# Optimization experiments

Hardware: AMD Instinct MI355X
Metric: run time of the kernel (lower is better)

The kernel has to match this reference:

```python
import jax, jax.numpy as jnp
import numpy as np

B, S, H = 4, 8192, 768
NH, HD = 12, 64          # num_heads, head_size
M = 64                   # projection_dim = min(256, HD)
EPS = 1e-6

def setup_inputs() -> dict:
    key = jax.random.key(0)
    ks = jax.random.split(key, 10)
    scale_w = 0.02
    scale_p = 1.0 / np.sqrt(HD)
    return {
        'hidden_states': jax.random.normal(ks[0], (B, S, H), jnp.float32),
        'Wq': jax.random.normal(ks[1], (H, H), jnp.float32) * scale_w,
        'bq': jnp.zeros((H,), jnp.float32),
        'Wk': jax.random.normal(ks[2], (H, H), jnp.float32) * scale_w,
        'bk': jnp.zeros((H,), jnp.float32),
        'Wv': jax.random.normal(ks[3], (H, H), jnp.float32) * scale_w,
        'bv': jnp.zeros((H,), jnp.float32),
        'Wo': jax.random.normal(ks[4], (H, H), jnp.float32) * scale_w,
        'bo': jnp.zeros((H,), jnp.float32),
        'projection_matrix': jax.random.normal(ks[5], (NH, HD, M), jnp.float32) * scale_p,
    }

def reference(hidden_states, Wq, bq, Wk, bk, Wv, bv, Wo, bo, projection_matrix):
    b, s, h = hidden_states.shape
    def heads(x):  # [b,s,h] -> [b,nh,s,hd]
        return x.reshape(b, s, NH, HD).transpose(0, 2, 1, 3)
    q = heads(hidden_states @ Wq + bq)
    k = heads(hidden_states @ Wk + bk)
    v = heads(hidden_states @ Wv + bv)
    # random-feature projection + stabilized exp feature map
    qp = jnp.einsum('bhnd,hdm->bhnm', q, projection_matrix)
    kp = jnp.einsum('bhnd,hdm->bhnm', k, projection_matrix)
    qp = jnp.exp(qp - jnp.max(qp, axis=-1, keepdims=True))
    kp = jnp.exp(kp - jnp.max(kp, axis=-1, keepdims=True))
    # O(n) linear attention: kv summary [b,h,m,hd]
    kv = jnp.einsum('bhnm,bhnd->bhmd', kp, v)
    qkv = jnp.einsum('bhnm,bhmd->bhnd', qp, kv)
    k_sum = jnp.sum(kp, axis=2)                      # [b,h,m]
    normalizer = jnp.einsum('bhnm,bhm->bhn', qp, k_sum)[..., None]
    ctx = qkv / (normalizer + EPS)
    ctx = ctx.transpose(0, 2, 1, 3).reshape(b, s, NH * HD)
    return ctx @ Wo + bo
```

## Files before the change

kernel.cpp:

```cpp
#include <hip/hip_runtime.h>
#include <hip/hip_bf16.h>


#define S_    8192
#define H_    768
#define NH_   12
#define EPS_  1e-6f

typedef unsigned short U16;
typedef short bf16x8 __attribute__((ext_vector_type(8)));
typedef float f32x4  __attribute__((ext_vector_type(4)));

__device__ __forceinline__ U16 f2b(float x) {
  unsigned u = __float_as_uint(x);
  return (U16)((u + 0x7fffu + ((u >> 16) & 1u)) >> 16);
}
__device__ __forceinline__ float b2f(U16 h) {
  return __uint_as_float(((unsigned)h) << 16);
}
__device__ __forceinline__ void gl2lds16(const void* g, void* l) {
  __builtin_amdgcn_global_load_lds(
      (const __attribute__((address_space(1))) void*)g,
      (__attribute__((address_space(3))) void*)l, 16, 0, 0);
}

__global__ void zero_f32(float* __restrict__ p, int n) {
  int i = blockIdx.x * 256 + threadIdx.x;
  if (i < n) p[i] = 0.f;
}

__global__ void cvt_f32_bf16(const float* __restrict__ src, U16* __restrict__ hi, int n4) {
  int i = blockIdx.x * 256 + threadIdx.x;
  if (i >= n4) return;
  float4 x = ((const float4*)src)[i];
  ushort4 h;
  h.x = f2b(x.x); h.y = f2b(x.y); h.z = f2b(x.z); h.w = f2b(x.w);
  ((ushort4*)hi)[i] = h;
}

__global__ void fold_proj(const float* __restrict__ Wq, const float* __restrict__ bq,
                          const float* __restrict__ Wk, const float* __restrict__ bk,
                          const float* __restrict__ P,
                          float* __restrict__ Wqp, float* __restrict__ bqp,
                          float* __restrict__ Wkp, float* __restrict__ bkp) {
  __shared__ float Pl[64 * 64];
  __shared__ float WL[4 * 64];
  int h = blockIdx.y, kc = blockIdx.x, tid = threadIdx.x;
  const float* W  = blockIdx.z ? Wk : Wq;
  const float* bb = blockIdx.z ? bk : bq;
  float* Wout = blockIdx.z ? Wkp : Wqp;
  float* bout = blockIdx.z ? bkp : bqp;
  const float4* P4 = (const float4*)(P + (size_t)h * 4096);
#pragma unroll
  for (int i = 0; i < 4; ++i) ((float4*)Pl)[tid + i * 256] = P4[tid + i * 256];
  WL[tid] = W[(size_t)(kc * 4 + (tid >> 6)) * H_ + h * 64 + (tid & 63)];
  __syncthreads();
  int kl = tid >> 6, m = tid & 63;
  float acc = 0.f;
#pragma unroll
  for (int d = 0; d < 64; ++d) acc += WL[kl * 64 + d] * Pl[d * 64 + m];
  Wout[(size_t)(kc * 4 + kl) * H_ + h * 64 + m] = acc;
  if (kc == 0 && tid < 64) {
    float a2 = 0.f;
    for (int d = 0; d < 64; ++d) a2 += bb[h * 64 + d] * Pl[d * 64 + tid];
    bout[h * 64 + tid] = a2;
  }
}

__global__ void build_cat(const float* __restrict__ Wqp, const float* __restrict__ Wkp,
                          const float* __restrict__ Wv,  const float* __restrict__ Wo,
                          U16* __restrict__ WcatH, U16* __restrict__ WoTH) {
  int k = blockIdx.x * 256 + threadIdx.x;
  int r = blockIdx.y;
  float v; U16* dh; size_t off;
  if (r < 768)       { v = Wqp[(size_t)k * H_ + r];          off = (size_t)r * H_ + k;          dh = WcatH; }
  else if (r < 1536) { v = Wkp[(size_t)k * H_ + (r - 768)];  off = (size_t)r * H_ + k;          dh = WcatH; }
  else if (r < 2304) { v = Wv [(size_t)k * H_ + (r - 1536)]; off = (size_t)r * H_ + k;          dh = WcatH; }
  else               { v = Wo [(size_t)k * H_ + (r - 2304)]; off = (size_t)(r - 2304) * H_ + k; dh = WoTH; }
  dh[off] = f2b(v);
}

__global__ void build_bias(const float* __restrict__ bqp, const float* __restrict__ bkp,
                           const float* __restrict__ bv, float* __restrict__ biasC) {
  int i = blockIdx.x * 256 + threadIdx.x;
  if (i >= 2304) return;
  biasC[i] = i < 768 ? bqp[i] : (i < 1536 ? bkp[i - 768] : bv[i - 1536]);
}

__global__ __launch_bounds__(256, 2) void gemm_qkv(
    const U16* __restrict__ Ahi, const U16* __restrict__ Bhi,
    const float* __restrict__ bias,
    U16* __restrict__ qp, U16* __restrict__ kpT, U16* __restrict__ vT) {
  __shared__ __align__(16) U16 Us[32768];
  const int tid = threadIdx.x, w = tid >> 6, lane = tid & 63;
  const int quad = lane >> 4, l16 = lane & 15;
  const int b = blockIdx.x;
  const int mt = b & 255, nt0 = b >> 8;
  const int rowA0 = mt * 128;
  const int wm = w & 1, wn = w >> 1;
  const U16* srcA[4];
  int rowBl[4];
  unsigned ldsc[4];
  const int kch = ((lane & 7) ^ (lane >> 3)) * 8;
#pragma unroll
  for (int t = 0; t < 4; ++t) {
    int c = w * 4 + t;
    int row = c * 8 + (lane >> 3);
    srcA[t] = Ahi + (size_t)(rowA0 + row) * H_ + kch;
    rowBl[t] = row;
    ldsc[t] = (unsigned)c * 512;
  }
  auto stage = [&](int jn, int tn, int bi) {
    const int colB = (nt0 + 2 * jn) * 128;
    unsigned ub = (unsigned)bi * 16384u;
#pragma unroll
    for (int t = 0; t < 4; ++t) {
      gl2lds16(srcA[t] + tn * 64, &Us[ub + ldsc[t]]);
      gl2lds16(Bhi + (size_t)(colB + rowBl[t]) * H_ + tn * 64 + kch,
               &Us[ub + 8192u + ldsc[t]]);
    }
  };

  stage(0, 0, 0);
  for (int jj = 0; jj < 9; ++jj) {
    const int colB0 = (nt0 + 2 * jj) * 128;
    f32x4 acc[4][4] = {};
    for (int t = 0; t < 12; ++t) {
      const bool more = !(jj == 8 && t == 11);
      if (more) {
        if (t < 11) stage(jj, t + 1, (t + 1) & 1);
        else        stage(jj + 1, 0, 0);
        asm volatile("s_waitcnt vmcnt(8)" ::: "memory");
      } else {
        asm volatile("s_waitcnt vmcnt(0)" ::: "memory");
      }
      __builtin_amdgcn_sched_barrier(0);
      __builtin_amdgcn_s_barrier();
      __builtin_amdgcn_sched_barrier(0);
      const unsigned ab = (unsigned)(t & 1) * 16384u;
      bf16x8 ah[4][2], bh[4][2];
#pragma unroll
      for (int i = 0; i < 4; ++i)
#pragma unroll
        for (int ks = 0; ks < 2; ++ks)
          ah[i][ks] = *(const bf16x8*)&Us[ab +
              (unsigned)((wm * 64 + i * 16 + l16) * 64 +
                         (((ks * 4 + quad) ^ (l16 & 7)) * 8))];
#pragma unroll
      for (int j = 0; j < 4; ++j)
#pragma unroll
        for (int ks = 0; ks < 2; ++ks)
          bh[j][ks] = *(const bf16x8*)&Us[ab + 8192u +
              (unsigned)((wn * 64 + j * 16 + l16) * 64 +
                         (((ks * 4 + quad) ^ (l16 & 7)) * 8))];
      asm volatile("s_waitcnt lgkmcnt(0)" ::: "memory");
      __builtin_amdgcn_sched_barrier(0);
      __builtin_amdgcn_s_setprio(1);
#pragma unroll
      for (int ks = 0; ks < 2; ++ks)
#pragma unroll
        for (int j = 0; j < 4; ++j)
#pragma unroll
          for (int i = 0; i < 4; ++i)
            acc[i][j] = __builtin_amdgcn_mfma_f32_16x16x32_bf16(
                ah[i][ks], bh[j][ks], acc[i][j], 0, 0, 0);
      __builtin_amdgcn_s_setprio(0);
      __builtin_amdgcn_sched_barrier(0);
      __builtin_amdgcn_s_barrier();
      __builtin_amdgcn_sched_barrier(0);
    }
    const int col64 = colB0 + wn * 64;
    float bj[4];
#pragma unroll
    for (int j = 0; j < 4; ++j) bj[j] = bias[col64 + j * 16 + l16];
    if (col64 < 768) {
      const int h = col64 >> 6;
#pragma unroll
      for (int i = 0; i < 4; ++i) {
#pragma unroll
        for (int r = 0; r < 4; ++r) {
          int row = rowA0 + wm * 64 + i * 16 + quad * 4 + r;
          float v0 = acc[i][0][r] + bj[0], v1 = acc[i][1][r] + bj[1];
          float v2 = acc[i][2][r] + bj[2], v3 = acc[i][3][r] + bj[3];
          float mx = fmaxf(fmaxf(v0, v1), fmaxf(v2, v3));
          mx = fmaxf(mx, __shfl_xor(mx, 1));
          mx = fmaxf(mx, __shfl_xor(mx, 2));
          mx = fmaxf(mx, __shfl_xor(mx, 4));
          mx = fmaxf(mx, __shfl_xor(mx, 8));
          int bb = row >> 13, s = row & 8191;
          size_t base = ((size_t)(bb * NH_ + h) * S_ + s) * 64 + l16;
          qp[base +  0] = f2b(__expf(v0 - mx));
          qp[base + 16] = f2b(__expf(v1 - mx));
          qp[base + 32] = f2b(__expf(v2 - mx));
          qp[base + 48] = f2b(__expf(v3 - mx));
        }
      }
    } else {
      const int isv = col64 >= 1536;
      const int h = (col64 - (isv ? 1536 : 768)) >> 6;
      U16* dstT = isv ? vT : kpT;
#pragma unroll
      for (int i = 0; i < 4; ++i) {
        float er[4][4];
#pragma unroll
        for (int r = 0; r < 4; ++r) {
          float v0 = acc[i][0][r] + bj[0], v1 = acc[i][1][r] + bj[1];
          float v2 = acc[i][2][r] + bj[2], v3 = acc[i][3][r] + bj[3];
          if (!isv) {
            float mx = fmaxf(fmaxf(v0, v1), fmaxf(v2, v3));
            mx = fmaxf(mx, __shfl_xor(mx, 1));
            mx = fmaxf(mx, __shfl_xor(mx, 2));
            mx = fmaxf(mx, __shfl_xor(mx, 4));
            mx = fmaxf(mx, __shfl_xor(mx, 8));
            v0 = __expf(v0 - mx); v1 = __expf(v1 - mx);
            v2 = __expf(v2 - mx); v3 = __expf(v3 - mx);
          }
          er[0][r] = v0; er[1][r] = v1; er[2][r] = v2; er[3][r] = v3;
        }
        int n = rowA0 + wm * 64 + i * 16 + quad * 4;
        int bb = n >> 13, s = n & 8191;
        int bh2 = bb * NH_ + h;
#pragma unroll
        for (int j = 0; j < 4; ++j) {
          ushort4 o;
          o.x = f2b(er[j][0]); o.y = f2b(er[j][1]);
          o.z = f2b(er[j][2]); o.w = f2b(er[j][3]);
          *(ushort4*)&dstT[((size_t)bh2 * 64 + j * 16 + l16) * S_ + s] = o;
        }
      }
    }
  }
}

__global__ __launch_bounds__(256, 4) void kv_accum_mfma(
    const U16* __restrict__ kpT, const U16* __restrict__ vT,
    float* __restrict__ kvT) {
  __shared__ __align__(16) U16 Us[2 * 64 * 64];
  const int tid = threadIdx.x, w = tid >> 6, lane = tid & 63;
  const int quad = lane >> 4, l16 = lane & 15;
  const int bh = blockIdx.y;
  const int n0 = blockIdx.x * 512;
  const U16* srcs[4];
  unsigned ldsoff[4];
#pragma unroll
  for (int t = 0; t < 4; ++t) {
    int c = w * 4 + t, buf = c >> 3;
    int r = (c & 7) * 8 + (lane >> 3);
    const U16* base = buf ? kpT : vT;
    srcs[t] = base + ((size_t)bh * 64 + r) * S_ + n0 + (lane & 7) * 8;
    ldsoff[t] = buf * 4096 + (c & 7) * 512;
  }
  f32x4 acc[4] = {};
  float ks[4] = {0.f, 0.f, 0.f, 0.f};
  for (int nc = 0; nc < 512; nc += 64) {
#pragma unroll
    for (int t = 0; t < 4; ++t) gl2lds16(srcs[t] + nc, &Us[ldsoff[t]]);
    __syncthreads();
#pragma unroll
    for (int k0 = 0; k0 < 64; k0 += 32) {
      bf16x8 av = *(const bf16x8*)&Us[(w * 16 + l16) * 64 + k0 + quad * 8];
#pragma unroll
      for (int j = 0; j < 4; ++j) {
        bf16x8 bk = *(const bf16x8*)&Us[4096 + (j * 16 + l16) * 64 + k0 + quad * 8];
        if (w == 0) {
#pragma unroll
          for (int e = 0; e < 8; ++e) ks[j] += b2f((U16)bk[e]);
        }
        acc[j] = __builtin_amdgcn_mfma_f32_16x16x32_bf16(av, bk, acc[j], 0, 0, 0);
      }
    }
    __syncthreads();
  }
#pragma unroll
  for (int j = 0; j < 4; ++j)
#pragma unroll
    for (int r = 0; r < 4; ++r) {
      int d = w * 16 + quad * 4 + r;
      atomicAdd(&kvT[((size_t)bh * 80 + d) * 64 + j * 16 + l16], acc[j][r]);
    }
  if (w == 0) {
#pragma unroll
    for (int j = 0; j < 4; ++j) {
      ks[j] += __shfl_xor(ks[j], 16);
      ks[j] += __shfl_xor(ks[j], 32);
    }
    if (lane < 16) {
#pragma unroll
      for (int j = 0; j < 4; ++j)
        atomicAdd(&kvT[((size_t)bh * 80 + 64) * 64 + j * 16 + lane], ks[j]);
    }
  }
}

#define CTXP 776
__global__ __launch_bounds__(256) void ctx_out(
    const U16* __restrict__ qp, const U16* __restrict__ kvH,
    const U16* __restrict__ WoTH, const float* __restrict__ bo,
    float* __restrict__ out) {
  extern __shared__ __align__(16) U16 smem[];
  U16* ctxL = smem;
  U16* WoTb = smem + 49664;
  const int tid = threadIdx.x, w = tid >> 6, lane = tid & 63;
  const int quad = lane >> 4, l16 = lane & 15;
  const int row0 = blockIdx.x * 64;
  const int bb = row0 >> 13, s0 = row0 & 8191;
  const int bh0 = bb * NH_;
#pragma unroll
  for (int h = 0; h < 12; ++h) {
    size_t qb = ((size_t)(bh0 + h) * S_ + s0 + w * 16 + l16) * 64;
    bf16x8 a0 = *(const bf16x8*)&qp[qb + quad * 8];
    bf16x8 a1 = *(const bf16x8*)&qp[qb + 32 + quad * 8];
    const U16* kb = kvH + (size_t)(bh0 + h) * 5120;
    f32x4 acc[5] = {};
#pragma unroll
    for (int j = 0; j < 5; ++j) {
      bf16x8 b0 = *(const bf16x8*)&kb[(j * 16 + l16) * 64 + quad * 8];
      bf16x8 b1 = *(const bf16x8*)&kb[(j * 16 + l16) * 64 + 32 + quad * 8];
      acc[j] = __builtin_amdgcn_mfma_f32_16x16x32_bf16(a0, b0, acc[j], 0, 0, 0);
      acc[j] = __builtin_amdgcn_mfma_f32_16x16x32_bf16(a1, b1, acc[j], 0, 0, 0);
    }
#pragma unroll
    for (int r = 0; r < 4; ++r) {
      float nv = __shfl(acc[4][r], lane & 48);
      float inv = 1.f / (nv + EPS_);
      int srow = w * 16 + quad * 4 + r;
#pragma unroll
      for (int j = 0; j < 4; ++j)
        ctxL[srow * CTXP + h * 64 + j * 16 + l16] = f2b(acc[j][r] * inv);
    }
  }
  __syncthreads();
  const int wm = w & 1, wn = w >> 1;
  const int kch = (((tid & 7) ^ ((tid >> 3) & 7)) * 8);
  auto stageW = [&](int tt, int bi) {
    int ntp = tt / 12, tp = tt - ntp * 12;
    const U16* src = WoTH + (size_t)(ntp * 128 + (tid >> 3)) * H_ + tp * 64 + kch;
    unsigned dst = (unsigned)bi * 8192u + (unsigned)tid * 8u;
#pragma unroll
    for (int k = 0; k < 4; ++k)
      gl2lds16(src + (size_t)(32 * k) * H_, &WoTb[dst + (unsigned)k * 2048u]);
  };
  stageW(0, 0);
  for (int nt = 0; nt < 6; ++nt) {
    f32x4 acc2[2][4] = {};
    for (int t = 0; t < 12; ++t) {
      int tt = nt * 12 + t;
      if (tt < 71) {
        stageW(tt + 1, (tt + 1) & 1);
        asm volatile("s_waitcnt vmcnt(4)" ::: "memory");
      } else {
        asm volatile("s_waitcnt vmcnt(0)" ::: "memory");
      }
      __builtin_amdgcn_sched_barrier(0);
      __builtin_amdgcn_s_barrier();
      __builtin_amdgcn_sched_barrier(0);
      const unsigned ab = (unsigned)(tt & 1) * 8192u;
      bf16x8 a2[2][2], b2[4][2];
#pragma unroll
      for (int i2 = 0; i2 < 2; ++i2)
#pragma unroll
        for (int ks = 0; ks < 2; ++ks)
          a2[i2][ks] = *(const bf16x8*)&ctxL[
              (wm * 32 + i2 * 16 + l16) * CTXP + t * 64 + ks * 32 + quad * 8];
#pragma unroll
      for (int j2 = 0; j2 < 4; ++j2)
#pragma unroll
        for (int ks = 0; ks < 2; ++ks)
          b2[j2][ks] = *(const bf16x8*)&WoTb[ab +
              (unsigned)((wn * 64 + j2 * 16 + l16) * 64 +
                         (((ks * 4 + quad) ^ (l16 & 7)) * 8))];
      asm volatile("s_waitcnt lgkmcnt(0)" ::: "memory");
      __builtin_amdgcn_sched_barrier(0);
      __builtin_amdgcn_s_setprio(1);
#pragma unroll
      for (int ks = 0; ks < 2; ++ks)
#pragma unroll
        for (int j2 = 0; j2 < 4; ++j2)
#pragma unroll
          for (int i2 = 0; i2 < 2; ++i2)
            acc2[i2][j2] = __builtin_amdgcn_mfma_f32_16x16x32_bf16(
                a2[i2][ks], b2[j2][ks], acc2[i2][j2], 0, 0, 0);
      __builtin_amdgcn_s_setprio(0);
      __builtin_amdgcn_sched_barrier(0);
      __builtin_amdgcn_s_barrier();
      __builtin_amdgcn_sched_barrier(0);
    }
#pragma unroll
    for (int i2 = 0; i2 < 2; ++i2) {
      int row = row0 + wm * 32 + i2 * 16 + quad * 4;
#pragma unroll
      for (int j2 = 0; j2 < 4; ++j2) {
        int col = nt * 128 + wn * 64 + j2 * 16 + l16;
        float bvv = bo[col];
#pragma unroll
        for (int r = 0; r < 4; ++r)
          out[(size_t)(row + r) * H_ + col] = acc2[i2][j2][r] + bvv;
      }
    }
  }
}

extern "C" void kernel_launch(void* const* d_in, const int* in_sizes, int n_in,
                              void* d_out, int out_size, void* d_ws, size_t ws_size,
                              hipStream_t stream) {
  const float* hs = (const float*)d_in[0];
  const float* Wq = (const float*)d_in[1];
  const float* bq = (const float*)d_in[2];
  const float* Wk = (const float*)d_in[3];
  const float* bk = (const float*)d_in[4];
  const float* Wv = (const float*)d_in[5];
  const float* bv = (const float*)d_in[6];
  const float* Wo = (const float*)d_in[7];
  const float* bo = (const float*)d_in[8];
  const float* P  = (const float*)d_in[9];
  float* out = (float*)d_out;

  char* ws = (char*)d_ws;
  size_t off = 0;
  auto alloc = [&](size_t bytes) -> void* {
    void* p = ws + off;
    off = (off + bytes + 255) & ~(size_t)255;
    return p;
  };
  U16*   hs_hi = (U16*)alloc(50331648);
  float* WqpF  = (float*)alloc(2359296);
  float* WkpF  = (float*)alloc(2359296);
  float* bqpF  = (float*)alloc(3072);
  float* bkpF  = (float*)alloc(3072);
  U16*   WcatH = (U16*)alloc(3538944);
  U16*   WoTH  = (U16*)alloc(1179648);
  float* biasC = (float*)alloc(9216);
  U16*   qp    = (U16*)alloc(50331648);
  U16*   kpT   = (U16*)alloc(50331648);
  U16*   vT    = (U16*)alloc(50331648);
  float* kvT   = (float*)alloc(983040);
  U16*   kvH   = (U16*)alloc(491520);

  zero_f32<<<dim3(960), dim3(256), 0, stream>>>(kvT, 245760);
  cvt_f32_bf16<<<dim3(24576), dim3(256), 0, stream>>>(hs, hs_hi, 6291456);
  fold_proj<<<dim3(192, 12, 2), dim3(256), 0, stream>>>(Wq, bq, Wk, bk, P, WqpF, bqpF, WkpF, bkpF);
  build_cat<<<dim3(3, 3072), dim3(256), 0, stream>>>(WqpF, WkpF, Wv, Wo, WcatH, WoTH);
  build_bias<<<dim3(9), dim3(256), 0, stream>>>(bqpF, bkpF, bv, biasC);
  gemm_qkv<<<dim3(512), dim3(256), 0, stream>>>(hs_hi, WcatH, biasC, qp, kpT, vT);
  kv_accum_mfma<<<dim3(16, 48), dim3(256), 0, stream>>>(kpT, vT, kvT);
  cvt_f32_bf16<<<dim3(240), dim3(256), 0, stream>>>(kvT, kvH, 61440);
  ctx_out<<<dim3(512), dim3(256), 132096, stream>>>(qp, kvH, WoTH, bo, out);
}
```

Before: 499.2 us.

## Fold kv summary into per-batch output weights and replace ctx_out with a plain GEMM

Instead of computing qp·kv per head and then multiplying by Wo, the kv summary of each batch is pre-multiplied into Wo to form per-batch combined weights (WKVT). The queries are normalized separately using a key sum that gemm_qkv now accumulates in its epilogue, and a simple 128x128 tile GEMM then produces the output directly. The weight transpose is also rewritten to use an LDS-tiled transpose. This removes the fused ctx_out kernel and its per-head MFMA plus LDS staging, but adds extra kernels, an extra bf16 write and read of a normalized qp tensor, and additional rounding through the bf16 combined weights.

Result: slower. 549.1 us (+10.0%).

```diff
diff --git a/kernel.cpp b/kernel.cpp
--- a/kernel.cpp
+++ b/kernel.cpp
@@ -67,17 +67,32 @@
   }
 }
 
-__global__ void build_cat(const float* __restrict__ Wqp, const float* __restrict__ Wkp,
-                          const float* __restrict__ Wv,  const float* __restrict__ Wo,
-                          U16* __restrict__ WcatH, U16* __restrict__ WoTH) {
-  int k = blockIdx.x * 256 + threadIdx.x;
-  int r = blockIdx.y;
-  float v; U16* dh; size_t off;
-  if (r < 768)       { v = Wqp[(size_t)k * H_ + r];          off = (size_t)r * H_ + k;          dh = WcatH; }
-  else if (r < 1536) { v = Wkp[(size_t)k * H_ + (r - 768)];  off = (size_t)r * H_ + k;          dh = WcatH; }
-  else if (r < 2304) { v = Wv [(size_t)k * H_ + (r - 1536)]; off = (size_t)r * H_ + k;          dh = WcatH; }
-  else               { v = Wo [(size_t)k * H_ + (r - 2304)]; off = (size_t)(r - 2304) * H_ + k; dh = WoTH; }
-  dh[off] = f2b(v);
+__global__ void build_cat_t(const float* __restrict__ Wqp, const float* __restrict__ Wkp,
+                            const float* __restrict__ Wv,  const float* __restrict__ Wo,
+                            U16* __restrict__ WcatH, U16* __restrict__ WoTH) {
+  __shared__ float T[64][68];
+  const int kb = blockIdx.x, rb = blockIdx.y, mat = blockIdx.z;
+  const int tid = threadIdx.x;
+  const float* W = mat == 0 ? Wqp : (mat == 1 ? Wkp : (mat == 2 ? Wv : Wo));
+#pragma unroll
+  for (int p = 0; p < 4; ++p) {
+    int idx = tid + p * 256;
+    int rr = idx >> 4, c4 = (idx & 15) * 4;
+    float4 v = *(const float4*)&W[(size_t)(kb * 64 + rr) * H_ + rb * 64 + c4];
+    T[rr][c4] = v.x; T[rr][c4 + 1] = v.y; T[rr][c4 + 2] = v.z; T[rr][c4 + 3] = v.w;
+  }
+  __syncthreads();
+  U16* dst = mat == 3 ? WoTH : WcatH;
+  const int rbase = (mat == 3 ? 0 : mat * 768) + rb * 64;
+#pragma unroll
+  for (int p = 0; p < 4; ++p) {
+    int idx = tid + p * 256;
+    int r2 = idx >> 4, c2 = (idx & 15) * 4;
+    ushort4 o;
+    o.x = f2b(T[c2 + 0][r2]); o.y = f2b(T[c2 + 1][r2]);
+    o.z = f2b(T[c2 + 2][r2]); o.w = f2b(T[c2 + 3][r2]);
+    *(ushort4*)&dst[(size_t)(rbase + r2) * H_ + kb * 64 + c2] = o;
+  }
 }
 
 __global__ void build_bias(const float* __restrict__ bqp, const float* __restrict__ bkp,
@@ -90,7 +105,8 @@
 __global__ __launch_bounds__(256, 2) void gemm_qkv(
     const U16* __restrict__ Ahi, const U16* __restrict__ Bhi,
     const float* __restrict__ bias,
-    U16* __restrict__ qp, U16* __restrict__ kpT, U16* __restrict__ vT) {
+    U16* __restrict__ qp, U16* __restrict__ kpT, U16* __restrict__ vT,
+    float* __restrict__ ksumF) {
   __shared__ __align__(16) U16 Us[32768];
   const int tid = threadIdx.x, w = tid >> 6, lane = tid & 63;
   const int quad = lane >> 4, l16 = lane & 15;
@@ -199,6 +215,8 @@
       const int isv = col64 >= 1536;
       const int h = (col64 - (isv ? 1536 : 768)) >> 6;
       U16* dstT = isv ? vT : kpT;
+      const int bh2 = (rowA0 >> 13) * NH_ + h;
+      float pk[4] = {0.f, 0.f, 0.f, 0.f};
 #pragma unroll
       for (int i = 0; i < 4; ++i) {
         float er[4][4];
@@ -217,9 +235,13 @@
           }
           er[0][r] = v0; er[1][r] = v1; er[2][r] = v2; er[3][r] = v3;
         }
+        if (!isv) {
+#pragma unroll
+          for (int j = 0; j < 4; ++j)
+            pk[j] += er[j][0] + er[j][1] + er[j][2] + er[j][3];
+        }
         int n = rowA0 + wm * 64 + i * 16 + quad * 4;
-        int bb = n >> 13, s = n & 8191;
-        int bh2 = bb * NH_ + h;
+        int s = n & 8191;
 #pragma unroll
         for (int j = 0; j < 4; ++j) {
           ushort4 o;
@@ -228,13 +250,25 @@
           *(ushort4*)&dstT[((size_t)bh2 * 64 + j * 16 + l16) * S_ + s] = o;
         }
       }
+      if (!isv) {
+#pragma unroll
+        for (int j = 0; j < 4; ++j) {
+          pk[j] += __shfl_xor(pk[j], 16);
+          pk[j] += __shfl_xor(pk[j], 32);
+        }
+        if (quad == 0) {
+#pragma unroll
+          for (int j = 0; j < 4; ++j)
+            atomicAdd(&ksumF[bh2 * 64 + j * 16 + l16], pk[j]);
+        }
+      }
     }
   }
 }
 
 __global__ __launch_bounds__(256, 4) void kv_accum_mfma(
     const U16* __restrict__ kpT, const U16* __restrict__ vT,
-    float* __restrict__ kvT) {
+    float* __restrict__ kvM) {
   __shared__ __align__(16) U16 Us[2 * 64 * 64];
   const int tid = threadIdx.x, w = tid >> 6, lane = tid & 63;
   const int quad = lane >> 4, l16 = lane & 15;
@@ -251,7 +285,6 @@
     ldsoff[t] = buf * 4096 + (c & 7) * 512;
   }
   f32x4 acc[4] = {};
-  float ks[4] = {0.f, 0.f, 0.f, 0.f};
   for (int nc = 0; nc < 512; nc += 64) {
 #pragma unroll
     for (int t = 0; t < 4; ++t) gl2lds16(srcs[t] + nc, &Us[ldsoff[t]]);
@@ -262,10 +295,6 @@
 #pragma unroll
       for (int j = 0; j < 4; ++j) {
         bf16x8 bk = *(const bf16x8*)&Us[4096 + (j * 16 + l16) * 64 + k0 + quad * 8];
-        if (w == 0) {
-#pragma unroll
-          for (int e = 0; e < 8; ++e) ks[j] += b2f((U16)bk[e]);
-        }
         acc[j] = __builtin_amdgcn_mfma_f32_16x16x32_bf16(av, bk, acc[j], 0, 0, 0);
       }
     }
@@ -274,128 +303,128 @@
 #pragma unroll
   for (int j = 0; j < 4; ++j)
 #pragma unroll
-    for (int r = 0; r < 4; ++r) {
-      int d = w * 16 + quad * 4 + r;
-      atomicAdd(&kvT[((size_t)bh * 80 + d) * 64 + j * 16 + l16], acc[j][r]);
-    }
-  if (w == 0) {
-#pragma unroll
-    for (int j = 0; j < 4; ++j) {
-      ks[j] += __shfl_xor(ks[j], 16);
-      ks[j] += __shfl_xor(ks[j], 32);
-    }
-    if (lane < 16) {
-#pragma unroll
-      for (int j = 0; j < 4; ++j)
-        atomicAdd(&kvT[((size_t)bh * 80 + 64) * 64 + j * 16 + lane], ks[j]);
-    }
-  }
-}
-
-#define CTXP 776
-__global__ __launch_bounds__(256) void ctx_out(
-    const U16* __restrict__ qp, const U16* __restrict__ kvH,
-    const U16* __restrict__ WoTH, const float* __restrict__ bo,
-    float* __restrict__ out) {
-  extern __shared__ __align__(16) U16 smem[];
-  U16* ctxL = smem;
-  U16* WoTb = smem + 49664;
+    for (int r = 0; r < 4; ++r)
+      atomicAdd(&kvM[((size_t)bh * 64 + j * 16 + l16) * 64 + w * 16 + quad * 4 + r],
+                acc[j][r]);
+}
+
+__global__ __launch_bounds__(256) void wkv_build(
+    const float* __restrict__ kvM, const U16* __restrict__ WoTH,
+    U16* __restrict__ WKVT) {
+  __shared__ float kvL[64][65];
+  __shared__ U16  WoL[128][66];
+  const int tid = threadIdx.x;
+  const int cB = blockIdx.x * 128, bh = blockIdx.y;
+  const int b = bh / NH_, h = bh - b * NH_;
+#pragma unroll
+  for (int p = 0; p < 16; ++p) {
+    int idx = tid + p * 256;
+    kvL[idx >> 6][idx & 63] = kvM[(size_t)bh * 4096 + idx];
+  }
+#pragma unroll
+  for (int p = 0; p < 32; ++p) {
+    int idx = tid + p * 256;
+    WoL[idx >> 6][idx & 63] = WoTH[(size_t)(cB + (idx >> 6)) * H_ + h * 64 + (idx & 63)];
+  }
+  __syncthreads();
+  const int c = tid & 127, m0 = (tid >> 7) * 32;
+  float acc[32] = {};
+  for (int d = 0; d < 64; ++d) {
+    float wv = b2f(WoL[c][d]);
+#pragma unroll
+    for (int mm = 0; mm < 32; ++mm) acc[mm] += wv * kvL[m0 + mm][d];
+  }
+  U16* dst = WKVT + (size_t)b * 589824 + (size_t)(cB + c) * H_ + h * 64 + m0;
+#pragma unroll
+  for (int mm = 0; mm < 32; mm += 4) {
+    ushort4 o;
+    o.x = f2b(acc[mm]); o.y = f2b(acc[mm + 1]);
+    o.z = f2b(acc[mm + 2]); o.w = f2b(acc[mm + 3]);
+    *(ushort4*)&dst[mm] = o;
+  }
+}
+
+__global__ __launch_bounds__(256) void qpn_scale(
+    const U16* __restrict__ qp, const float* __restrict__ ksumF,
+    U16* __restrict__ ctx) {
+  __shared__ float ks[64];
+  const int tid = threadIdx.x;
+  const int bh = blockIdx.y, s0 = blockIdx.x * 64;
+  if (tid < 64) ks[tid] = ksumF[bh * 64 + tid];
+  __syncthreads();
+  const int row = tid >> 2, q = tid & 3;
+  size_t src = ((size_t)bh * S_ + s0 + row) * 64 + q * 16;
+  bf16x8 x0 = *(const bf16x8*)&qp[src];
+  bf16x8 x1 = *(const bf16x8*)&qp[src + 8];
+  float f[16];
+  float n = 0.f;
+#pragma unroll
+  for (int e = 0; e < 8; ++e) {
+    f[e] = b2f((U16)x0[e]);     n += f[e] * ks[q * 16 + e];
+    f[e + 8] = b2f((U16)x1[e]); n += f[e + 8] * ks[q * 16 + 8 + e];
+  }
+  n += __shfl_xor(n, 1);
+  n += __shfl_xor(n, 2);
+  const float inv = 1.f / (n + EPS_);
+  const int b = bh / NH_, h = bh - b * NH_;
+  U16* dst = ctx + ((size_t)(b * S_ + s0 + row)) * H_ + h * 64 + q * 16;
+#pragma unroll
+  for (int g = 0; g < 4; ++g) {
+    ushort4 o;
+    o.x = f2b(f[g * 4 + 0] * inv); o.y = f2b(f[g * 4 + 1] * inv);
+    o.z = f2b(f[g * 4 + 2] * inv); o.w = f2b(f[g * 4 + 3] * inv);
+    *(ushort4*)&dst[g * 4] = o;
+  }
+}
+
+__global__ __launch_bounds__(256, 4) void out_gemm(
+    const U16* __restrict__ Ahi, const U16* __restrict__ WKVT,
+    const float* __restrict__ bias, float* __restrict__ C) {
+  __shared__ __align__(16) U16 Us[2 * 128 * 32];
   const int tid = threadIdx.x, w = tid >> 6, lane = tid & 63;
   const int quad = lane >> 4, l16 = lane & 15;
-  const int row0 = blockIdx.x * 64;
-  const int bb = row0 >> 13, s0 = row0 & 8191;
-  const int bh0 = bb * NH_;
-#pragma unroll
-  for (int h = 0; h < 12; ++h) {
-    size_t qb = ((size_t)(bh0 + h) * S_ + s0 + w * 16 + l16) * 64;
-    bf16x8 a0 = *(const bf16x8*)&qp[qb + quad * 8];
-    bf16x8 a1 = *(const bf16x8*)&qp[qb + 32 + quad * 8];
-    const U16* kb = kvH + (size_t)(bh0 + h) * 5120;
-    f32x4 acc[5] = {};
-#pragma unroll
-    for (int j = 0; j < 5; ++j) {
-      bf16x8 b0 = *(const bf16x8*)&kb[(j * 16 + l16) * 64 + quad * 8];
-      bf16x8 b1 = *(const bf16x8*)&kb[(j * 16 + l16) * 64 + 32 + quad * 8];
-      acc[j] = __builtin_amdgcn_mfma_f32_16x16x32_bf16(a0, b0, acc[j], 0, 0, 0);
-      acc[j] = __builtin_amdgcn_mfma_f32_16x16x32_bf16(a1, b1, acc[j], 0, 0, 0);
-    }
-#pragma unroll
-    for (int r = 0; r < 4; ++r) {
-      float nv = __shfl(acc[4][r], lane & 48);
-      float inv = 1.f / (nv + EPS_);
-      int srow = w * 16 + quad * 4 + r;
-#pragma unroll
-      for (int j = 0; j < 4; ++j)
-        ctxL[srow * CTXP + h * 64 + j * 16 + l16] = f2b(acc[j][r] * inv);
-    }
-  }
-  __syncthreads();
+  const int rowA0 = blockIdx.y * 128, colB0 = blockIdx.x * 128;
   const int wm = w & 1, wn = w >> 1;
-  const int kch = (((tid & 7) ^ ((tid >> 3) & 7)) * 8);
-  auto stageW = [&](int tt, int bi) {
-    int ntp = tt / 12, tp = tt - ntp * 12;
-    const U16* src = WoTH + (size_t)(ntp * 128 + (tid >> 3)) * H_ + tp * 64 + kch;
-    unsigned dst = (unsigned)bi * 8192u + (unsigned)tid * 8u;
-#pragma unroll
-    for (int k = 0; k < 4; ++k)
-      gl2lds16(src + (size_t)(32 * k) * H_, &WoTb[dst + (unsigned)k * 2048u]);
-  };
-  stageW(0, 0);
-  for (int nt = 0; nt < 6; ++nt) {
-    f32x4 acc2[2][4] = {};
-    for (int t = 0; t < 12; ++t) {
-      int tt = nt * 12 + t;
-      if (tt < 71) {
-        stageW(tt + 1, (tt + 1) & 1);
-        asm volatile("s_waitcnt vmcnt(4)" ::: "memory");
-      } else {
-        asm volatile("s_waitcnt vmcnt(0)" ::: "memory");
-      }
-      __builtin_amdgcn_sched_barrier(0);
-      __builtin_amdgcn_s_barrier();
-      __builtin_amdgcn_sched_barrier(0);
-      const unsigned ab = (unsigned)(tt & 1) * 8192u;
-      bf16x8 a2[2][2], b2[4][2];
-#pragma unroll
-      for (int i2 = 0; i2 < 2; ++i2)
-#pragma unroll
-        for (int ks = 0; ks < 2; ++ks)
-          a2[i2][ks] = *(const bf16x8*)&ctxL[
-              (wm * 32 + i2 * 16 + l16) * CTXP + t * 64 + ks * 32 + quad * 8];
-#pragma unroll
-      for (int j2 = 0; j2 < 4; ++j2)
-#pragma unroll
-        for (int ks = 0; ks < 2; ++ks)
-          b2[j2][ks] = *(const bf16x8*)&WoTb[ab +
-              (unsigned)((wn * 64 + j2 * 16 + l16) * 64 +
-                         (((ks * 4 + quad) ^ (l16 & 7)) * 8))];
-      asm volatile("s_waitcnt lgkmcnt(0)" ::: "memory");
-      __builtin_amdgcn_sched_barrier(0);
-      __builtin_amdgcn_s_setprio(1);
-#pragma unroll
-      for (int ks = 0; ks < 2; ++ks)
-#pragma unroll
-        for (int j2 = 0; j2 < 4; ++j2)
-#pragma unroll
-          for (int i2 = 0; i2 < 2; ++i2)
-            acc2[i2][j2] = __builtin_amdgcn_mfma_f32_16x16x32_bf16(
-                a2[i2][ks], b2[j2][ks], acc2[i2][j2], 0, 0, 0);
-      __builtin_amdgcn_s_setprio(0);
-      __builtin_amdgcn_sched_barrier(0);
-      __builtin_amdgcn_s_barrier();
-      __builtin_amdgcn_sched_barrier(0);
-    }
-#pragma unroll
-    for (int i2 = 0; i2 < 2; ++i2) {
-      int row = row0 + wm * 32 + i2 * 16 + quad * 4;
-#pragma unroll
-      for (int j2 = 0; j2 < 4; ++j2) {
-        int col = nt * 128 + wn * 64 + j2 * 16 + l16;
-        float bvv = bo[col];
-#pragma unroll
-        for (int r = 0; r < 4; ++r)
-          out[(size_t)(row + r) * H_ + col] = acc2[i2][j2][r] + bvv;
-      }
+  const int K = 768;
+  const U16* Bb = WKVT + (size_t)(blockIdx.y >> 6) * 589824;
+  f32x4 acc[4][4] = {};
+  const U16* srcs[4];
+  unsigned ldsoff[4];
+#pragma unroll
+  for (int t = 0; t < 4; ++t) {
+    int c = w * 4 + t, cc = c & 7, buf = c >> 3;
+    const U16* base = buf ? Bb : Ahi;
+    int r0 = buf ? colB0 : rowA0;
+    srcs[t] = base + (size_t)(r0 + cc * 16 + (lane >> 2)) * K + (lane & 3) * 8;
+    ldsoff[t] = c * 512;
+  }
+  for (int k0 = 0; k0 < K; k0 += 32) {
+#pragma unroll
+    for (int t = 0; t < 4; ++t) gl2lds16(srcs[t] + k0, &Us[ldsoff[t]]);
+    __syncthreads();
+    bf16x8 ah[4];
+#pragma unroll
+    for (int i = 0; i < 4; ++i)
+      ah[i] = *(const bf16x8*)&Us[(wm * 64 + i * 16 + l16) * 32 + quad * 8];
+#pragma unroll
+    for (int j = 0; j < 4; ++j) {
+      bf16x8 bh = *(const bf16x8*)&Us[4096 + (wn * 64 + j * 16 + l16) * 32 + quad * 8];
+#pragma unroll
+      for (int i = 0; i < 4; ++i)
+        acc[i][j] = __builtin_amdgcn_mfma_f32_16x16x32_bf16(ah[i], bh, acc[i][j], 0, 0, 0);
+    }
+    __syncthreads();
+  }
+#pragma unroll
+  for (int i = 0; i < 4; ++i) {
+    int row = rowA0 + wm * 64 + i * 16 + quad * 4;
+#pragma unroll
+    for (int j = 0; j < 4; ++j) {
+      int col = colB0 + wn * 64 + j * 16 + l16;
+      float bvv = bias[col];
+#pragma unroll
+      for (int r = 0; r < 4; ++r)
+        C[(size_t)(row + r) * H_ + col] = acc[i][j][r] + bvv;
     }
   }
 }
@@ -433,16 +462,19 @@
   U16*   qp    = (U16*)alloc(50331648);
   U16*   kpT   = (U16*)alloc(50331648);
   U16*   vT    = (U16*)alloc(50331648);
-  float* kvT   = (float*)alloc(983040);
-  U16*   kvH   = (U16*)alloc(491520);
-
-  zero_f32<<<dim3(960), dim3(256), 0, stream>>>(kvT, 245760);
+  float* kvM   = (float*)alloc(786432);
+  float* ksumF = (float*)alloc(12288);
+  U16*   WKVT  = (U16*)alloc(4718592);
+  U16*   ctx   = hs_hi;
+
+  zero_f32<<<dim3(780), dim3(256), 0, stream>>>(kvM, 199680);
   cvt_f32_bf16<<<dim3(24576), dim3(256), 0, stream>>>(hs, hs_hi, 6291456);
   fold_proj<<<dim3(192, 12, 2), dim3(256), 0, stream>>>(Wq, bq, Wk, bk, P, WqpF, bqpF, WkpF, bkpF);
-  build_cat<<<dim3(3, 3072), dim3(256), 0, stream>>>(WqpF, WkpF, Wv, Wo, WcatH, WoTH);
+  build_cat_t<<<dim3(12, 12, 4), dim3(256), 0, stream>>>(WqpF, WkpF, Wv, Wo, WcatH, WoTH);
   build_bias<<<dim3(9), dim3(256), 0, stream>>>(bqpF, bkpF, bv, biasC);
-  gemm_qkv<<<dim3(512), dim3(256), 0, stream>>>(hs_hi, WcatH, biasC, qp, kpT, vT);
-  kv_accum_mfma<<<dim3(16, 48), dim3(256), 0, stream>>>(kpT, vT, kvT);
-  cvt_f32_bf16<<<dim3(240), dim3(256), 0, stream>>>(kvT, kvH, 61440);
-  ctx_out<<<dim3(512), dim3(256), 132096, stream>>>(qp, kvH, WoTH, bo, out);
-}
+  gemm_qkv<<<dim3(512), dim3(256), 0, stream>>>(hs_hi, WcatH, biasC, qp, kpT, vT, ksumF);
+  kv_accum_mfma<<<dim3(16, 48), dim3(256), 0, stream>>>(kpT, vT, kvM);
+  wkv_build<<<dim3(6, 48), dim3(256), 0, stream>>>(kvM, WoTH, WKVT);
+  qpn_scale<<<dim3(128, 48), dim3(256), 0, stream>>>(qp, ksumF, ctx);
+  out_gemm<<<dim3(6, 256), dim3(256), 0, stream>>>(ctx, WKVT, bo, out);
+}
```
